# Optimization experiments

Measured on AMD Instinct MI355X. Metric: run time of the kernel, lower is better.

Reference implementation:

```python
import jax, jax.numpy as jnp
import numpy as np

NUM_HEADS = 16
NUM_KV_HEADS = 4
HEAD_DIM = 128
BASE_THETA = 10000.0


def _rope_cos_sin(seq_len, head_dim, dtype):
    # standard (ntk_alpha=1) rotate-half RoPE tables: [S, head_dim]
    inv_freq = 1.0 / (BASE_THETA ** (jnp.arange(0, head_dim, 2, dtype=jnp.float32) / head_dim))
    angles = jnp.arange(seq_len, dtype=jnp.float32)[:, None] * inv_freq[None, :]  # [S, D/2]
    cos = jnp.concatenate([jnp.cos(angles), jnp.cos(angles)], axis=-1).astype(dtype)
    sin = jnp.concatenate([jnp.sin(angles), jnp.sin(angles)], axis=-1).astype(dtype)
    return cos, sin


def _rotate_half(t):
    half = t.shape[-1] // 2
    return jnp.concatenate([-t[..., half:], t[..., :half]], axis=-1)


def setup_inputs() -> dict:
    key = jax.random.key(0)
    ks = jax.random.split(key, 5)
    B, S, E = 2, 2048, 2048
    KV = NUM_KV_HEADS * HEAD_DIM  # 512
    scale = 0.02
    return {
        "x": jax.random.normal(ks[0], (B, S, E), dtype=jnp.float32),
        "Wq": jax.random.normal(ks[1], (E, E), dtype=jnp.float32) * scale,
        "Wk": jax.random.normal(ks[2], (E, KV), dtype=jnp.float32) * scale,
        "Wv": jax.random.normal(ks[3], (E, KV), dtype=jnp.float32) * scale,
        "Wo": jax.random.normal(ks[4], (E, E), dtype=jnp.float32) * scale,
    }


def reference(x, Wq, Wk, Wv, Wo):
    B, S, E = x.shape
    n_rep = NUM_HEADS // NUM_KV_HEADS
    scale = 1.0 / jnp.sqrt(jnp.float32(HEAD_DIM))

    # QKV projections (bias=False)
    q = (x @ Wq).reshape(B, S, NUM_HEADS, HEAD_DIM)
    k = (x @ Wk).reshape(B, S, NUM_KV_HEADS, HEAD_DIM)
    v = (x @ Wv).reshape(B, S, NUM_KV_HEADS, HEAD_DIM)

    # dynamic RoPE on q, k
    cos, sin = _rope_cos_sin(S, HEAD_DIM, x.dtype)
    cos = cos[None, :, None, :]
    sin = sin[None, :, None, :]
    q = q * cos + _rotate_half(q) * sin
    k = k * cos + _rotate_half(k) * sin

    # GQA: repeat kv heads to match query heads
    k = jnp.repeat(k, n_rep, axis=2)
    v = jnp.repeat(v, n_rep, axis=2)

    # [B, H, S, D]
    q = q.transpose(0, 2, 1, 3)
    k = k.transpose(0, 2, 1, 3)
    v = v.transpose(0, 2, 1, 3)

    # causal mask (window_size=0 -> standard causal, additive float mask)
    i = jnp.arange(S)[:, None]
    j = jnp.arange(S)[None, :]
    neg = jnp.finfo(jnp.float32).min
    causal = jnp.where(j > i, neg, 0.0).astype(jnp.float32)  # [S, S]

    scores = jnp.einsum("bhqd,bhkd->bhqk", q, k) * scale
    scores = scores + causal[None, None, :, :]
    weights = jax.nn.softmax(scores.astype(jnp.float32), axis=-1)
    attn = jnp.einsum("bhqk,bhkd->bhqd", weights.astype(v.dtype), v)

    attn = attn.transpose(0, 2, 1, 3).reshape(B, S, E)
    return attn @ Wo
```

## Files before the change

kernel.cpp:

```cpp
#include <hip/hip_runtime.h>
#include <math.h>


typedef __attribute__((ext_vector_type(8))) short short8;
typedef __attribute__((ext_vector_type(4))) float f32x4;
typedef __attribute__((ext_vector_type(16))) float f32x16;

typedef const __attribute__((address_space(1))) void* gvp;
typedef __attribute__((address_space(3))) void* svp;

__device__ __forceinline__ void async16(const void* g, void* l) {
  __builtin_amdgcn_global_load_lds((gvp)g, (svp)l, 16, 0, 0);
}
__device__ __forceinline__ void wait_vm0() { asm volatile("s_waitcnt vmcnt(0)" ::: "memory"); }
__device__ __forceinline__ void barrier_raw() { asm volatile("s_barrier" ::: "memory"); }

__device__ __forceinline__ unsigned short f2b(float f) {
  unsigned int u = __builtin_bit_cast(unsigned int, f);
  u += 0x7fffu + ((u >> 16) & 1u);
  return (unsigned short)(u >> 16);
}
__device__ __forceinline__ float b2f(unsigned short h) {
  unsigned int u = ((unsigned int)h) << 16;
  return __builtin_bit_cast(float, u);
}

__device__ __forceinline__ unsigned int pk_bf16(float a, float b) {
  unsigned int r;
  asm("v_cvt_pk_bf16_f32 %0, %1, %2" : "=v"(r) : "v"(a), "v"(b));
  return r;
}
__device__ __forceinline__ void plswap(unsigned int& a, unsigned int& b) {
  asm("v_permlane32_swap_b32 %0, %1" : "+v"(a), "+v"(b));
}

__global__ __launch_bounds__(256) void prep(const float* __restrict__ x,
                                            const float* __restrict__ Wq,
                                            const float* __restrict__ Wk,
                                            const float* __restrict__ Wv,
                                            const float* __restrict__ Wo,
                                            unsigned short* __restrict__ xb,
                                            unsigned short* __restrict__ WqkvT,
                                            unsigned short* __restrict__ WoT) {
  __shared__ float t[32][33];
  if (blockIdx.x < 4096) {
    int i = blockIdx.x * 256 + threadIdx.x;
    const float4* p = (const float4*)x + (size_t)i * 2;
    float4 a = p[0], b4 = p[1];
    union { short8 v; unsigned short u[8]; } o;
    o.u[0] = f2b(a.x);  o.u[1] = f2b(a.y);  o.u[2] = f2b(a.z);  o.u[3] = f2b(a.w);
    o.u[4] = f2b(b4.x); o.u[5] = f2b(b4.y); o.u[6] = f2b(b4.z); o.u[7] = f2b(b4.w);
    ((short8*)xb)[i] = o.v;
    return;
  }
  int idx = blockIdx.x - 4096;
  const float* W; unsigned short* WT; int N, tx, ty;
  const int K = 2048;
  if (idx < 4096)      { W = Wq; WT = WqkvT;                         N = 2048; idx -= 0;    tx = idx & 63; ty = idx >> 6; }
  else if (idx < 5120) { W = Wk; WT = WqkvT + (size_t)2048 * 2048;   N = 512;  idx -= 4096; tx = idx & 15; ty = idx >> 4; }
  else if (idx < 6144) { W = Wv; WT = WqkvT + (size_t)2560 * 2048;   N = 512;  idx -= 5120; tx = idx & 15; ty = idx >> 4; }
  else                 { W = Wo; WT = WoT;                           N = 2048; idx -= 6144; tx = idx & 63; ty = idx >> 6; }
  int c = threadIdx.x & 31, r0 = threadIdx.x >> 5;
  int k0 = ty * 32, n0 = tx * 32;
#pragma unroll
  for (int r = r0; r < 32; r += 8) t[r][c] = W[(size_t)(k0 + r) * N + n0 + c];
  __syncthreads();
#pragma unroll
  for (int r = r0; r < 32; r += 8) WT[(size_t)(n0 + r) * K + k0 + c] = f2b(t[c][r]);
}

__global__ __launch_bounds__(256) void gemm_bt(const unsigned short* __restrict__ A,
                                               const unsigned short* __restrict__ BT,
                                               void* __restrict__ Cout,
                                               int M, int N, int K, int out_bf16) {
  const int n0 = blockIdx.x * 128;
  const int m0 = blockIdx.y * 128;
  const int tid = threadIdx.x;
  const int w = tid >> 6, lane = tid & 63, l15 = lane & 15, quad = lane >> 4;
  const int wm = w >> 1, wn = w & 1;

  __shared__ __align__(16) unsigned short As[2][128 * 64];
  __shared__ __align__(16) unsigned short Bs[2][128 * 64];

  f32x4 acc[4][4];
#pragma unroll
  for (int mi = 0; mi < 4; mi++)
#pragma unroll
    for (int ni = 0; ni < 4; ni++) acc[mi][ni] = (f32x4){0.f, 0.f, 0.f, 0.f};

  const int rl = lane >> 3;
  const int cl = lane & 7;
  const unsigned short* Ab = A + (size_t)m0 * K;
  const unsigned short* Bb = BT + (size_t)n0 * K;

#pragma unroll
  for (int i = 0; i < 4; i++) {
    int row = w * 32 + i * 8 + rl;
    int gc = cl ^ (row & 7);
    async16(Ab + (size_t)row * K + gc * 8, &As[0][(w * 32 + i * 8) * 64]);
    async16(Bb + (size_t)row * K + gc * 8, &Bs[0][(w * 32 + i * 8) * 64]);
  }

  const int nIter = K >> 6;
  for (int j = 0; j < nIter; j++) {
    wait_vm0();
    barrier_raw();
    const int cur = j & 1;

    if (j + 1 < nIter) {
      int kb = (j + 1) * 64;
#pragma unroll
      for (int i = 0; i < 4; i++) {
        int row = w * 32 + i * 8 + rl;
        int gc = cl ^ (row & 7);
        async16(Ab + (size_t)row * K + kb + gc * 8, &As[cur ^ 1][(w * 32 + i * 8) * 64]);
        async16(Bb + (size_t)row * K + kb + gc * 8, &Bs[cur ^ 1][(w * 32 + i * 8) * 64]);
      }
    }

    const unsigned short* as = &As[cur][0];
    const unsigned short* bs = &Bs[cur][0];
#pragma unroll
    for (int kk = 0; kk < 2; kk++) {
      short8 af[4], bfv[4];
#pragma unroll
      for (int mi = 0; mi < 4; mi++) {
        int row = wm * 64 + mi * 16 + l15;
        af[mi] = *(const short8*)&as[row * 64 + (((kk * 4 + quad) ^ (row & 7)) * 8)];
      }
#pragma unroll
      for (int ni = 0; ni < 4; ni++) {
        int row = wn * 64 + ni * 16 + l15;
        bfv[ni] = *(const short8*)&bs[row * 64 + (((kk * 4 + quad) ^ (row & 7)) * 8)];
      }
#pragma unroll
      for (int mi = 0; mi < 4; mi++)
#pragma unroll
        for (int ni = 0; ni < 4; ni++)
          acc[mi][ni] = __builtin_amdgcn_mfma_f32_16x16x32_bf16(af[mi], bfv[ni],
                                                                acc[mi][ni], 0, 0, 0);
    }
  }

  if (out_bf16) {
    unsigned short* C = (unsigned short*)Cout;
#pragma unroll
    for (int mi = 0; mi < 4; mi++)
#pragma unroll
      for (int ni = 0; ni < 4; ni++)
#pragma unroll
        for (int r = 0; r < 4; r++) {
          int row = m0 + wm * 64 + mi * 16 + quad * 4 + r;
          int col = n0 + wn * 64 + ni * 16 + l15;
          C[(size_t)row * N + col] = f2b(acc[mi][ni][r]);
        }
  } else {
    float* C = (float*)Cout;
#pragma unroll
    for (int mi = 0; mi < 4; mi++)
#pragma unroll
      for (int ni = 0; ni < 4; ni++)
#pragma unroll
        for (int r = 0; r < 4; r++) {
          int row = m0 + wm * 64 + mi * 16 + quad * 4 + r;
          int col = n0 + wn * 64 + ni * 16 + l15;
          C[(size_t)row * N + col] = acc[mi][ni][r];
        }
  }
}

#define SC_TOT 0.12753785056274918f
__global__ __launch_bounds__(256) void gemm_qkv(const unsigned short* __restrict__ A,
                                                const unsigned short* __restrict__ BT,
                                                unsigned short* __restrict__ Qm,
                                                unsigned short* __restrict__ Km,
                                                unsigned short* __restrict__ Vtm) {
  const int N = 3072, K = 2048;
  const int n0 = blockIdx.x * 128;
  const int m0 = blockIdx.y * 128;
  const int tid = threadIdx.x;
  const int w = tid >> 6, lane = tid & 63, l15 = lane & 15, quad = lane >> 4;
  const int wm = w >> 1, wn = w & 1;

  __shared__ __align__(16) unsigned char smem[65536];
  unsigned short (*As)[128 * 64] = (unsigned short (*)[128 * 64])smem;
  unsigned short (*Bs)[128 * 64] = (unsigned short (*)[128 * 64])(smem + 32768);
  float* L = (float*)smem;

  f32x4 acc[4][4];
#pragma unroll
  for (int mi = 0; mi < 4; mi++)
#pragma unroll
    for (int ni = 0; ni < 4; ni++) acc[mi][ni] = (f32x4){0.f, 0.f, 0.f, 0.f};

  const int rl = lane >> 3;
  const int cl = lane & 7;
  const unsigned short* Ab = A + (size_t)m0 * K;
  const unsigned short* Bb = BT + (size_t)n0 * K;

#pragma unroll
  for (int i = 0; i < 4; i++) {
    int row = w * 32 + i * 8 + rl;
    int gc = cl ^ (row & 7);
    async16(Ab + (size_t)row * K + gc * 8, &As[0][(w * 32 + i * 8) * 64]);
    async16(Bb + (size_t)row * K + gc * 8, &Bs[0][(w * 32 + i * 8) * 64]);
  }

  const int nIter = K >> 6;
  for (int j = 0; j < nIter; j++) {
    wait_vm0();
    barrier_raw();
    const int cur = j & 1;

    if (j + 1 < nIter) {
      int kb = (j + 1) * 64;
#pragma unroll
      for (int i = 0; i < 4; i++) {
        int row = w * 32 + i * 8 + rl;
        int gc = cl ^ (row & 7);
        async16(Ab + (size_t)row * K + kb + gc * 8, &As[cur ^ 1][(w * 32 + i * 8) * 64]);
        async16(Bb + (size_t)row * K + kb + gc * 8, &Bs[cur ^ 1][(w * 32 + i * 8) * 64]);
      }
    }

    const unsigned short* as = &As[cur][0];
    const unsigned short* bs = &Bs[cur][0];
#pragma unroll
    for (int kk = 0; kk < 2; kk++) {
      short8 af[4], bfv[4];
#pragma unroll
      for (int mi = 0; mi < 4; mi++) {
        int row = wm * 64 + mi * 16 + l15;
        af[mi] = *(const short8*)&as[row * 64 + (((kk * 4 + quad) ^ (row & 7)) * 8)];
      }
#pragma unroll
      for (int ni = 0; ni < 4; ni++) {
        int row = wn * 64 + ni * 16 + l15;
        bfv[ni] = *(const short8*)&bs[row * 64 + (((kk * 4 + quad) ^ (row & 7)) * 8)];
      }
#pragma unroll
      for (int mi = 0; mi < 4; mi++)
#pragma unroll
        for (int ni = 0; ni < 4; ni++)
          acc[mi][ni] = __builtin_amdgcn_mfma_f32_16x16x32_bf16(af[mi], bfv[ni],
                                                                acc[mi][ni], 0, 0, 0);
    }
  }

  __syncthreads();
#pragma unroll
  for (int mi = 0; mi < 4; mi++)
#pragma unroll
    for (int ni = 0; ni < 4; ni++)
#pragma unroll
      for (int r = 0; r < 4; r++) {
        int rr = wm * 64 + mi * 16 + quad * 4 + r;
        int cc = wn * 64 + ni * 16 + l15;
        L[rr * 128 + (cc ^ (rr & 31))] = acc[mi][ni][r];
      }
  __syncthreads();

  const int head = blockIdx.x;
  const int b = m0 >> 11;
  const int s_base = m0 & 2047;

  if (head < 20) {
    const int d = tid & 63, sl = tid >> 6;
    const bool isQ = head < 16;
    unsigned short* dq = isQ
      ? Qm + ((size_t)((b * 16 + head) * 2048 + s_base)) * 128
      : Km + ((size_t)((b * 4 + (head - 16)) * 2048 + s_base)) * 128;
    const float invf = exp2f(-0.20762050593046f * (float)d);
#pragma unroll 4
    for (int i = 0; i < 32; i++) {
      int s = sl + i * 4;
      float lo = b2f(f2b(L[s * 128 + (d ^ (s & 31))]));
      float hi = b2f(f2b(L[s * 128 + ((d + 64) ^ (s & 31))]));
      float ang = (float)(s_base + s) * invf;
      float sn, cs;
      sincosf(ang, &sn, &cs);
      float nlo = lo * cs - hi * sn;
      float nhi = hi * cs + lo * sn;
      if (isQ) { nlo *= SC_TOT; nhi *= SC_TOT; }
      dq[(size_t)s * 128 + d]      = f2b(nlo);
      dq[(size_t)s * 128 + d + 64] = f2b(nhi);
    }
  } else {
    const int kv = head - 20;
    const int s_l = tid & 63, dl = tid >> 6;
    unsigned short* dv = Vtm + ((size_t)(b * 4 + kv) * 128) * 2048;
#pragma unroll 2
    for (int sh = 0; sh < 2; sh++) {
      int s = sh * 64 + s_l;
#pragma unroll 4
      for (int i = 0; i < 32; i++) {
        int d = i * 4 + dl;
        dv[(size_t)d * 2048 + s_base + s] = f2b(L[s * 128 + (d ^ (s & 31))]);
      }
    }
  }
}

#define FIXED_M 12.0f

__device__ __forceinline__ void proc_acc(const f32x16& s, bool msk, int kvb, int q,
                                         float& l_own, short8& paL, short8& paH) {
  float p[16];
#pragma unroll
  for (int r = 0; r < 16; r++) {
    float v = exp2f(s[r] - FIXED_M);
    if (msk) {
      int kv = kvb + (r & 3) + 8 * (r >> 2);
      if (kv > q) v = 0.f;
    }
    p[r] = v;
    l_own += v;
  }
  unsigned int u0 = pk_bf16(p[0], p[1]),  u1 = pk_bf16(p[2], p[3]);
  unsigned int u2 = pk_bf16(p[4], p[5]),  u3 = pk_bf16(p[6], p[7]);
  plswap(u0, u2); plswap(u1, u3);
  unsigned int w0 = pk_bf16(p[8], p[9]),  w1 = pk_bf16(p[10], p[11]);
  unsigned int w2 = pk_bf16(p[12], p[13]), w3 = pk_bf16(p[14], p[15]);
  plswap(w0, w2); plswap(w1, w3);
  union { unsigned int u[4]; short8 s8; } a, b;
  a.u[0] = u0; a.u[1] = u1; a.u[2] = u2; a.u[3] = u3;
  b.u[0] = w0; b.u[1] = w1; b.u[2] = w2; b.u[3] = w3;
  paL = a.s8; paH = b.s8;
}

__global__ __launch_bounds__(512, 2) void flash2(const unsigned short* __restrict__ Q,
                                                 const unsigned short* __restrict__ Kc,
                                                 const unsigned short* __restrict__ Vt,
                                                 unsigned short* __restrict__ attn) {
  const int pair = blockIdx.x;
  const int h = blockIdx.y;
  const int b = blockIdx.z;
  const int kvh = h >> 2;
  const int tid = threadIdx.x;
  const int w = tid >> 6;
  const int g = w >> 2;
  const int wg = w & 3;
  const int lane = tid & 63;
  const int l31 = lane & 31, hi = lane >> 5, x7 = l31 & 7;

  __shared__ __align__(16) unsigned short kbuf[2][2][64 * 128];
  __shared__ __align__(16) unsigned short vbuf[2][2][128 * 64];
  __shared__ float lx[2][4][32];
  __shared__ float li[2][4][32];

  const unsigned short* Qb = Q  + ((size_t)(b * 16 + h)) * 2048 * 128;
  const unsigned short* Kb = Kc + ((size_t)(b * 4 + kvh)) * 2048 * 128;
  const unsigned short* Vb = Vt + ((size_t)(b * 4 + kvh)) * 128 * 2048;

  for (int t = 0; t < 2; t++) {
    const int qt = (t == 0) ? pair : (15 - pair);
    const int q0 = qt * 128;
    const int qw = q0 + wg * 32;
    const int qv = qw + l31;
    const int half = qt + 1;
    const int j0 = g * half;

    short8 qf[8];
    {
      const unsigned short* qp = Qb + (size_t)qv * 128 + hi * 8;
#pragma unroll
      for (int s = 0; s < 8; s++) qf[s] = *(const short8*)(qp + s * 16);
    }

    f32x16 o[4];
#pragma unroll
    for (int d = 0; d < 4; d++)
#pragma unroll
      for (int e = 0; e < 16; e++) o[d][e] = 0.f;
    float l_own = 0.f;

    __syncthreads();

#pragma unroll
    for (int k2 = 0; k2 < 4; k2++) {
      int m = wg * 4 + k2;
      int rl = m * 4 + (lane >> 4);
      int c8 = (lane & 15) ^ (rl & 7);
      async16(Kb + (size_t)(j0 * 64 + rl) * 128 + c8 * 8, &kbuf[g][0][m * 512]);
    }
#pragma unroll
    for (int k2 = 0; k2 < 4; k2++) {
      int m = wg * 4 + k2;
      int d = m * 8 + (lane >> 3);
      int c3 = (lane & 7) ^ (d & 7);
      async16(Vb + (size_t)d * 2048 + j0 * 64 + c3 * 8, &vbuf[g][0][m * 512]);
    }

    for (int i = 0; i < half; i++) {
      wait_vm0();
      barrier_raw();
      const int cur = i & 1;
      const int kb = (j0 + i) * 64;

      if (i + 1 < half) {
        int kb2 = kb + 64;
#pragma unroll
        for (int k2 = 0; k2 < 4; k2++) {
          int m = wg * 4 + k2;
          int rl = m * 4 + (lane >> 4);
          int c8 = (lane & 15) ^ (rl & 7);
          async16(Kb + (size_t)(kb2 + rl) * 128 + c8 * 8, &kbuf[g][cur ^ 1][m * 512]);
        }
#pragma unroll
        for (int k2 = 0; k2 < 4; k2++) {
          int m = wg * 4 + k2;
          int d = m * 8 + (lane >> 3);
          int c3 = (lane & 7) ^ (d & 7);
          async16(Vb + (size_t)d * 2048 + kb2 + c3 * 8, &vbuf[g][cur ^ 1][m * 512]);
        }
      }

      if (kb <= qw + 31) {
        f32x16 sA, sB;
#pragma unroll
        for (int e = 0; e < 16; e++) { sA[e] = 0.f; sB[e] = 0.f; }
        const unsigned short* kp = &kbuf[g][cur][0];
        __builtin_amdgcn_s_setprio(1);
#pragma unroll
        for (int s = 0; s < 8; s++) {
          int ch = (((s << 1) | hi) ^ x7) << 3;
          short8 ka = *(const short8*)&kp[l31 * 128 + ch];
          short8 kB2 = *(const short8*)&kp[(32 + l31) * 128 + ch];
          sA = __builtin_amdgcn_mfma_f32_32x32x16_bf16(ka, qf[s], sA, 0, 0, 0);
          sB = __builtin_amdgcn_mfma_f32_32x32x16_bf16(kB2, qf[s], sB, 0, 0, 0);
        }
        __builtin_amdgcn_s_setprio(0);

        const bool msk = (kb + 63 > qw);
        short8 pa[4];
        proc_acc(sA, msk, kb + 4 * hi, qv, l_own, pa[0], pa[1]);
        proc_acc(sB, msk, kb + 32 + 4 * hi, qv, l_own, pa[2], pa[3]);

        const unsigned short* vp = &vbuf[g][cur][0];
        __builtin_amdgcn_s_setprio(1);
#pragma unroll
        for (int db = 0; db < 4; db++) {
          int ro = (db * 32 + l31) * 64;
#pragma unroll
          for (int f = 0; f < 4; f++) {
            int ch = (((f << 1) | hi) ^ x7) << 3;
            short8 vf = *(const short8*)&vp[ro + ch];
            o[db] = __builtin_amdgcn_mfma_f32_32x32x16_bf16(pa[f], vf, o[db], 0, 0, 0);
          }
        }
        __builtin_amdgcn_s_setprio(0);
      }
    }

    __syncthreads();
    {
      float* wout = (float*)&kbuf[g ^ 1][0][0];
      float lown = l_own + __shfl_xor(l_own, 32);
      if (hi == 0) lx[g][wg][l31] = lown;
      const int base = wg * 2048 + lane * 4;
      if (g == 0) {
#pragma unroll
        for (int r4 = 0; r4 < 4; r4++) {
          *(f32x4*)&wout[base + 0 * 1024 + r4 * 256] =
            (f32x4){ o[2][r4 * 4 + 0], o[2][r4 * 4 + 1], o[2][r4 * 4 + 2], o[2][r4 * 4 + 3] };
          *(f32x4*)&wout[base + 1 * 1024 + r4 * 256] =
            (f32x4){ o[3][r4 * 4 + 0], o[3][r4 * 4 + 1], o[3][r4 * 4 + 2], o[3][r4 * 4 + 3] };
        }
      } else {
#pragma unroll
        for (int r4 = 0; r4 < 4; r4++) {
          *(f32x4*)&wout[base + 0 * 1024 + r4 * 256] =
            (f32x4){ o[0][r4 * 4 + 0], o[0][r4 * 4 + 1], o[0][r4 * 4 + 2], o[0][r4 * 4 + 3] };
          *(f32x4*)&wout[base + 1 * 1024 + r4 * 256] =
            (f32x4){ o[1][r4 * 4 + 0], o[1][r4 * 4 + 1], o[1][r4 * 4 + 2], o[1][r4 * 4 + 3] };
        }
      }
      __syncthreads();
      const float* rin = (const float*)&kbuf[g][0][0];
      float ltot = lown + lx[g ^ 1][wg][l31];
      if (hi == 0) li[g][wg][l31] = 1.f / ltot;
      f32x4 inv4[4];
#pragma unroll
      for (int tt = 0; tt < 4; tt++) inv4[tt] = *(const f32x4*)&li[g][wg][tt * 8 + 4 * hi];

      unsigned short* ap0 = attn + ((size_t)(b * 2048 + qw)) * 2048 + h * 128 + l31;
      if (g == 0) {
#pragma unroll
        for (int r4 = 0; r4 < 4; r4++) {
          f32x4 v0 = *(const f32x4*)&rin[base + 0 * 1024 + r4 * 256];
          f32x4 v1 = *(const f32x4*)&rin[base + 1 * 1024 + r4 * 256];
#pragma unroll
          for (int k = 0; k < 4; k++) {
            o[0][r4 * 4 + k] += v0[k];
            o[1][r4 * 4 + k] += v1[k];
          }
        }
#pragma unroll
        for (int r = 0; r < 16; r++) {
          int rowq = (r & 3) + 8 * (r >> 2) + 4 * hi;
          float iv = inv4[r >> 2][r & 3];
          ap0[(size_t)rowq * 2048 + 0]  = f2b(o[0][r] * iv);
          ap0[(size_t)rowq * 2048 + 32] = f2b(o[1][r] * iv);
        }
      } else {
#pragma unroll
        for (int r4 = 0; r4 < 4; r4++) {
          f32x4 v0 = *(const f32x4*)&rin[base + 0 * 1024 + r4 * 256];
          f32x4 v1 = *(const f32x4*)&rin[base + 1 * 1024 + r4 * 256];
#pragma unroll
          for (int k = 0; k < 4; k++) {
            o[2][r4 * 4 + k] += v0[k];
            o[3][r4 * 4 + k] += v1[k];
          }
        }
#pragma unroll
        for (int r = 0; r < 16; r++) {
          int rowq = (r & 3) + 8 * (r >> 2) + 4 * hi;
          float iv = inv4[r >> 2][r & 3];
          ap0[(size_t)rowq * 2048 + 64] = f2b(o[2][r] * iv);
          ap0[(size_t)rowq * 2048 + 96] = f2b(o[3][r] * iv);
        }
      }
    }
  }
}

extern "C" void kernel_launch(void* const* d_in, const int* in_sizes, int n_in,
                              void* d_out, int out_size, void* d_ws, size_t ws_size,
                              hipStream_t stream) {
  const float* x  = (const float*)d_in[0];
  const float* Wq = (const float*)d_in[1];
  const float* Wk = (const float*)d_in[2];
  const float* Wv = (const float*)d_in[3];
  const float* Wo = (const float*)d_in[4];
  float* out = (float*)d_out;

  char* ws = (char*)d_ws;
  unsigned short* xb    = (unsigned short*)(ws);
  unsigned short* WqkvT = (unsigned short*)(ws + 16777216);
  unsigned short* WoT   = (unsigned short*)(ws + 29360128);
  unsigned short* Qm    = (unsigned short*)(ws + 62914560);
  unsigned short* Km    = (unsigned short*)(ws + 79691776);
  unsigned short* Vtm   = (unsigned short*)(ws + 83886080);
  unsigned short* attn  = xb;

  prep<<<14336, 256, 0, stream>>>(x, Wq, Wk, Wv, Wo, xb, WqkvT, WoT);

  gemm_qkv<<<dim3(24, 32), 256, 0, stream>>>(xb, WqkvT, Qm, Km, Vtm);

  flash2<<<dim3(8, 16, 2), 512, 0, stream>>>(Qm, Km, Vtm, attn);

  gemm_bt<<<dim3(16, 32), 256, 0, stream>>>(attn, WoT, out, 4096, 2048, 2048, 0);
}
```

Before: 307.4 us.

## Use four-stage K=32 async LDS pipeline with partial vmcnt waits in GEMMs

```diff
diff --git a/kernel.cpp b/kernel.cpp
--- a/kernel.cpp
+++ b/kernel.cpp
@@ -13,6 +13,8 @@
   __builtin_amdgcn_global_load_lds((gvp)g, (svp)l, 16, 0, 0);
 }
 __device__ __forceinline__ void wait_vm0() { asm volatile("s_waitcnt vmcnt(0)" ::: "memory"); }
+__device__ __forceinline__ void wait_vm4() { asm volatile("s_waitcnt vmcnt(4)" ::: "memory"); }
+__device__ __forceinline__ void wait_vm8() { asm volatile("s_waitcnt vmcnt(8)" ::: "memory"); }
 __device__ __forceinline__ void barrier_raw() { asm volatile("s_barrier" ::: "memory"); }
 
 __device__ __forceinline__ unsigned short f2b(float f) {
@@ -69,6 +71,43 @@
   for (int r = r0; r < 32; r += 8) WT[(size_t)(n0 + r) * K + k0 + c] = f2b(t[c][r]);
 }
 
+#define GQ_STAGE(J, BUF)                                                      \
+  { int kb_ = (J) * 32;                                                       \
+    _Pragma("unroll") for (int i = 0; i < 2; ++i) {                           \
+      int row = w * 32 + i * 16 + (lane >> 2);                                \
+      int gc = (lane & 3) ^ (row & 3);                                        \
+      async16(Ab + (size_t)row * K + kb_ + gc * 8,                            \
+              &As[BUF][(w * 32 + i * 16) * 32]);                              \
+      async16(Bb + (size_t)row * K + kb_ + gc * 8,                            \
+              &Bs[BUF][(w * 32 + i * 16) * 32]); } }
+
+#define GQ_COMPUTE(CUR)                                                       \
+  { const unsigned short* as_ = &As[CUR][0];                                  \
+    const unsigned short* bs_ = &Bs[CUR][0];                                  \
+    short8 af[4], bfv[4];                                                     \
+    _Pragma("unroll") for (int mi = 0; mi < 4; ++mi) {                        \
+      int row = wm * 64 + mi * 16 + l15;                                      \
+      af[mi] = *(const short8*)&as_[row * 32 + ((quad ^ (row & 3)) * 8)]; }   \
+    _Pragma("unroll") for (int ni = 0; ni < 4; ++ni) {                        \
+      int row = wn * 64 + ni * 16 + l15;                                      \
+      bfv[ni] = *(const short8*)&bs_[row * 32 + ((quad ^ (row & 3)) * 8)]; }  \
+    _Pragma("unroll") for (int mi = 0; mi < 4; ++mi)                          \
+      _Pragma("unroll") for (int ni = 0; ni < 4; ++ni)                        \
+        acc[mi][ni] = __builtin_amdgcn_mfma_f32_16x16x32_bf16(                \
+            af[mi], bfv[ni], acc[mi][ni], 0, 0, 0); }
+
+#define GQ_LOOP                                                               \
+  GQ_STAGE(0, 0); GQ_STAGE(1, 1); GQ_STAGE(2, 2);                             \
+  const int nIter = K >> 5;                                                   \
+  for (int j = 0; j < nIter; ++j) {                                           \
+    if (j + 2 < nIter) wait_vm8();                                            \
+    else if (j + 1 < nIter) wait_vm4();                                       \
+    else wait_vm0();                                                          \
+    barrier_raw();                                                            \
+    if (j + 3 < nIter) GQ_STAGE(j + 3, (j + 3) & 3);                          \
+    GQ_COMPUTE(j & 3);                                                        \
+  }
+
 __global__ __launch_bounds__(256) void gemm_bt(const unsigned short* __restrict__ A,
                                                const unsigned short* __restrict__ BT,
                                                void* __restrict__ Cout,
@@ -79,8 +118,8 @@
   const int w = tid >> 6, lane = tid & 63, l15 = lane & 15, quad = lane >> 4;
   const int wm = w >> 1, wn = w & 1;
 
-  __shared__ __align__(16) unsigned short As[2][128 * 64];
-  __shared__ __align__(16) unsigned short Bs[2][128 * 64];
+  __shared__ __align__(16) unsigned short As[4][128 * 32];
+  __shared__ __align__(16) unsigned short Bs[4][128 * 32];
 
   f32x4 acc[4][4];
 #pragma unroll
@@ -88,59 +127,10 @@
 #pragma unroll
     for (int ni = 0; ni < 4; ni++) acc[mi][ni] = (f32x4){0.f, 0.f, 0.f, 0.f};
 
-  const int rl = lane >> 3;
-  const int cl = lane & 7;
   const unsigned short* Ab = A + (size_t)m0 * K;
   const unsigned short* Bb = BT + (size_t)n0 * K;
 
-#pragma unroll
-  for (int i = 0; i < 4; i++) {
-    int row = w * 32 + i * 8 + rl;
-    int gc = cl ^ (row & 7);
-    async16(Ab + (size_t)row * K + gc * 8, &As[0][(w * 32 + i * 8) * 64]);
-    async16(Bb + (size_t)row * K + gc * 8, &Bs[0][(w * 32 + i * 8) * 64]);
-  }
-
-  const int nIter = K >> 6;
-  for (int j = 0; j < nIter; j++) {
-    wait_vm0();
-    barrier_raw();
-    const int cur = j & 1;
-
-    if (j + 1 < nIter) {
-      int kb = (j + 1) * 64;
-#pragma unroll
-      for (int i = 0; i < 4; i++) {
-        int row = w * 32 + i * 8 + rl;
-        int gc = cl ^ (row & 7);
-        async16(Ab + (size_t)row * K + kb + gc * 8, &As[cur ^ 1][(w * 32 + i * 8) * 64]);
-        async16(Bb + (size_t)row * K + kb + gc * 8, &Bs[cur ^ 1][(w * 32 + i * 8) * 64]);
-      }
-    }
-
-    const unsigned short* as = &As[cur][0];
-    const unsigned short* bs = &Bs[cur][0];
-#pragma unroll
-    for (int kk = 0; kk < 2; kk++) {
-      short8 af[4], bfv[4];
-#pragma unroll
-      for (int mi = 0; mi < 4; mi++) {
-        int row = wm * 64 + mi * 16 + l15;
-        af[mi] = *(const short8*)&as[row * 64 + (((kk * 4 + quad) ^ (row & 7)) * 8)];
-      }
-#pragma unroll
-      for (int ni = 0; ni < 4; ni++) {
-        int row = wn * 64 + ni * 16 + l15;
-        bfv[ni] = *(const short8*)&bs[row * 64 + (((kk * 4 + quad) ^ (row & 7)) * 8)];
-      }
-#pragma unroll
-      for (int mi = 0; mi < 4; mi++)
-#pragma unroll
-        for (int ni = 0; ni < 4; ni++)
-          acc[mi][ni] = __builtin_amdgcn_mfma_f32_16x16x32_bf16(af[mi], bfv[ni],
-                                                                acc[mi][ni], 0, 0, 0);
-    }
-  }
+  GQ_LOOP
 
   if (out_bf16) {
     unsigned short* C = (unsigned short*)Cout;
@@ -175,7 +165,7 @@
                                                 unsigned short* __restrict__ Qm,
                                                 unsigned short* __restrict__ Km,
                                                 unsigned short* __restrict__ Vtm) {
-  const int N = 3072, K = 2048;
+  const int K = 2048;
   const int n0 = blockIdx.x * 128;
   const int m0 = blockIdx.y * 128;
   const int tid = threadIdx.x;
@@ -183,8 +173,8 @@
   const int wm = w >> 1, wn = w & 1;
 
   __shared__ __align__(16) unsigned char smem[65536];
-  unsigned short (*As)[128 * 64] = (unsigned short (*)[128 * 64])smem;
-  unsigned short (*Bs)[128 * 64] = (unsigned short (*)[128 * 64])(smem + 32768);
+  unsigned short (*As)[128 * 32] = (unsigned short (*)[128 * 32])smem;
+  unsigned short (*Bs)[128 * 32] = (unsigned short (*)[128 * 32])(smem + 32768);
   float* L = (float*)smem;
 
   f32x4 acc[4][4];
@@ -193,59 +183,10 @@
 #pragma unroll
     for (int ni = 0; ni < 4; ni++) acc[mi][ni] = (f32x4){0.f, 0.f, 0.f, 0.f};
 
-  const int rl = lane >> 3;
-  const int cl = lane & 7;
   const unsigned short* Ab = A + (size_t)m0 * K;
   const unsigned short* Bb = BT + (size_t)n0 * K;
 
-#pragma unroll
-  for (int i = 0; i < 4; i++) {
-    int row = w * 32 + i * 8 + rl;
-    int gc = cl ^ (row & 7);
-    async16(Ab + (size_t)row * K + gc * 8, &As[0][(w * 32 + i * 8) * 64]);
-    async16(Bb + (size_t)row * K + gc * 8, &Bs[0][(w * 32 + i * 8) * 64]);
-  }
-
-  const int nIter = K >> 6;
-  for (int j = 0; j < nIter; j++) {
-    wait_vm0();
-    barrier_raw();
-    const int cur = j & 1;
-
-    if (j + 1 < nIter) {
-      int kb = (j + 1) * 64;
-#pragma unroll
-      for (int i = 0; i < 4; i++) {
-        int row = w * 32 + i * 8 + rl;
-        int gc = cl ^ (row & 7);
-        async16(Ab + (size_t)row * K + kb + gc * 8, &As[cur ^ 1][(w * 32 + i * 8) * 64]);
-        async16(Bb + (size_t)row * K + kb + gc * 8, &Bs[cur ^ 1][(w * 32 + i * 8) * 64]);
-      }
-    }
-
-    const unsigned short* as = &As[cur][0];
-    const unsigned short* bs = &Bs[cur][0];
-#pragma unroll
-    for (int kk = 0; kk < 2; kk++) {
-      short8 af[4], bfv[4];
-#pragma unroll
-      for (int mi = 0; mi < 4; mi++) {
-        int row = wm * 64 + mi * 16 + l15;
-        af[mi] = *(const short8*)&as[row * 64 + (((kk * 4 + quad) ^ (row & 7)) * 8)];
-      }
-#pragma unroll
-      for (int ni = 0; ni < 4; ni++) {
-        int row = wn * 64 + ni * 16 + l15;
-        bfv[ni] = *(const short8*)&bs[row * 64 + (((kk * 4 + quad) ^ (row & 7)) * 8)];
-      }
-#pragma unroll
-      for (int mi = 0; mi < 4; mi++)
-#pragma unroll
-        for (int ni = 0; ni < 4; ni++)
-          acc[mi][ni] = __builtin_amdgcn_mfma_f32_16x16x32_bf16(af[mi], bfv[ni],
-                                                                acc[mi][ni], 0, 0, 0);
-    }
-  }
+  GQ_LOOP
 
   __syncthreads();
 #pragma unroll
```

After: 308.2 us. No clear change (+0.3%).
